# Kernel optimization log

Measured on AMD Instinct MI355X. Metric: run time of the kernel, lower is better.

Reference implementation:

```python
import jax, jax.numpy as jnp
import numpy as np

B, L, D, H = 2, 2048, 2048, 16
C = D // H  # head dim = 128
EPS = 1e-5


def setup_inputs() -> dict:
    key = jax.random.key(0)
    k1, k2, k3, k4 = jax.random.split(key, 4)
    scale = 1.0 / np.sqrt(D)
    return {
        "x": jax.random.normal(k1, (B, L, D), dtype=jnp.float32),
        "theta": jax.random.uniform(k2, (B, L, D // 2), dtype=jnp.float32) * 6.2831853,
        "w_qkv": jax.random.normal(k3, (3 * D, D), dtype=jnp.float32) * scale,
        "w_y": jax.random.normal(k4, (D, D), dtype=jnp.float32) * scale,
        "b_y": jnp.zeros((D,), dtype=jnp.float32),
    }


def _rms_norm(t):
    # RMSNorm over last dim, eps=1e-5, no affine
    return t * jax.lax.rsqrt(jnp.mean(t * t, axis=-1, keepdims=True) + EPS)


def _apply_rope(q, k, theta):
    # q, k: (B, H, L, C); theta: (B, H, L, C//2)
    qr, qi = q[..., 0::2], q[..., 1::2]
    kr, ki = k[..., 0::2], k[..., 1::2]
    cos_t, sin_t = jnp.cos(theta), jnp.sin(theta)
    q_rot = jnp.stack((qr * cos_t - qi * sin_t, qr * sin_t + qi * cos_t), axis=-1).reshape(q.shape)
    k_rot = jnp.stack((kr * cos_t - ki * sin_t, kr * sin_t + ki * cos_t), axis=-1).reshape(k.shape)
    return q_rot, k_rot


def reference(x, theta, w_qkv, w_y, b_y):
    # QKV projection: (B, L, 3D)
    qkv = jnp.einsum("bld,ed->ble", x, w_qkv)
    # rearrange '... L (n H C) -> n ... H L C'
    qkv = qkv.reshape(B, L, 3, H, C).transpose(2, 0, 3, 1, 4)  # (3, B, H, L, C)
    q, k, v = qkv[0], qkv[1], qkv[2]
    q, k = _rms_norm(q), _rms_norm(k)
    # theta: (B, L, H*C/2) -> (B, H, L, C/2)
    th = theta.reshape(B, L, H, C // 2).transpose(0, 2, 1, 3)
    q, k = _apply_rope(q, k, th)
    # scaled dot-product attention
    scores = jnp.einsum("bhqc,bhkc->bhqk", q, k) / np.sqrt(C).astype(np.float32)
    attn = jax.nn.softmax(scores, axis=-1)
    y = jnp.einsum("bhqk,bhkc->bhqc", attn, v)
    # (B, H, L, C) -> (B, L, H*C)
    y = y.transpose(0, 2, 1, 3).reshape(B, L, D)
    return jnp.einsum("bld,ed->ble", y, w_y) + b_y
```

## Files before the change

kernel.cpp:

```cpp
#include <hip/hip_runtime.h>
#include <stdint.h>

typedef uint16_t u16;
typedef __attribute__((ext_vector_type(8))) short bf16x8;
typedef __attribute__((ext_vector_type(4))) float f32x4;


__device__ __forceinline__ u16 f2bf(float f) {
  uint32_t u = __builtin_bit_cast(uint32_t, f);
  u += 0x7fffu + ((u >> 16) & 1u);
  return (u16)(u >> 16);
}
__device__ __forceinline__ float bf2f(u16 h) {
  return __builtin_bit_cast(float, (uint32_t)h << 16);
}
__device__ __forceinline__ uint32_t pack2bf(float a, float b) {
  uint32_t ua = __builtin_bit_cast(uint32_t, a) + 0x7fffu;
  uint32_t ub = __builtin_bit_cast(uint32_t, b) + 0x7fffu;
  return (ua >> 16) | (ub & 0xffff0000u);
}
__device__ __forceinline__ void gl_lds16(const u16* g, u16* l) {
  __builtin_amdgcn_global_load_lds((const __attribute__((address_space(1))) uint32_t*)g,
                                   (__attribute__((address_space(3))) uint32_t*)l, 16, 0, 0);
}

__global__ __launch_bounds__(256) void castk(const float* __restrict__ in,
                                             u16* __restrict__ out, int n) {
  int idx = (blockIdx.x * 256 + threadIdx.x) * 4;
  int stride = gridDim.x * 256 * 4;
  for (int i = idx; i < n; i += stride) {
    float4 v = *(const float4*)(in + i);
    uint32_t lo = (uint32_t)f2bf(v.x) | ((uint32_t)f2bf(v.y) << 16);
    uint32_t hi = (uint32_t)f2bf(v.z) | ((uint32_t)f2bf(v.w) << 16);
    *(uint2*)(out + i) = make_uint2(lo, hi);
  }
}

__global__ __launch_bounds__(512, 1) void gemm8_qkv(
    const u16* __restrict__ A, const u16* __restrict__ Bw,
    u16* __restrict__ qb, u16* __restrict__ kb, u16* __restrict__ vt) {
  __shared__ u16 sm[57344];
  const int K = 2048;
  const int tid = threadIdx.x, lane = tid & 63;
  const int wid = tid >> 6, g = lane >> 4, lr = lane & 15;
  const int wm = wid >> 2, wn = wid & 3;
  const int m0 = blockIdx.y * 256, n0 = blockIdx.x * 192;
  const int srow = tid >> 3, sjs = (tid & 7) ^ (srow & 7);

  auto stA = [&](int buf, int kt, int R) {
    gl_lds16(A + (size_t)(m0 + R + srow) * K + kt * 64 + sjs * 8,
             &sm[buf * 28672 + R * 64 + tid * 8]);
  };
  auto stB = [&](int buf, int kt, int R) {
    gl_lds16(Bw + (size_t)(n0 + R + srow) * K + kt * 64 + sjs * 8,
             &sm[buf * 28672 + 16384 + R * 64 + tid * 8]);
  };
  auto rdA = [&](const u16* As, int mf, int ks) {
    int ra = wm * 128 + mf * 16 + lr;
    return *(const bf16x8*)&As[ra * 64 + (((ks * 4 + g) ^ (ra & 7)) * 8)];
  };
  auto rdB = [&](const u16* Bs, int nf, int ks) {
    int rb = wn * 48 + nf * 16 + lr;
    return *(const bf16x8*)&Bs[rb * 64 + (((ks * 4 + g) ^ (rb & 7)) * 8)];
  };

  f32x4 acc[8][3] = {};
  bf16x8 bc[3][2], fP0[4][2], fP1[4][2];

  stB(0, 0, 0); stB(0, 0, 64); stB(0, 0, 128);
  stA(0, 0, 0); stA(0, 0, 128);
  stA(0, 0, 64); stA(0, 0, 192);
  asm volatile("s_waitcnt vmcnt(2)" ::: "memory");
  __builtin_amdgcn_s_barrier();
  {
    const u16* As0 = &sm[0];
#pragma unroll
    for (int i = 0; i < 4; ++i)
#pragma unroll
      for (int ks = 0; ks < 2; ++ks) fP0[i][ks] = rdA(As0, i, ks);
  }

  for (int t = 0; t < 32; ++t) {
    const int cur = t & 1, nxt = cur ^ 1;
    const int kn = (t < 31) ? t + 1 : 31;
    const u16* Asc = &sm[cur * 28672];
    const u16* Bsc = &sm[cur * 28672 + 16384];
    const u16* Asn = &sm[nxt * 28672];

    stB(nxt, kn, 0); stB(nxt, kn, 64); stB(nxt, kn, 128);
    stA(nxt, kn, 0); stA(nxt, kn, 128);
    asm volatile("s_waitcnt vmcnt(5)" ::: "memory");
    __builtin_amdgcn_s_barrier();
#pragma unroll
    for (int nf = 0; nf < 3; ++nf)
#pragma unroll
      for (int ks = 0; ks < 2; ++ks) bc[nf][ks] = rdB(Bsc, nf, ks);
#pragma unroll
    for (int i = 0; i < 4; ++i)
#pragma unroll
      for (int ks = 0; ks < 2; ++ks) fP1[i][ks] = rdA(Asc, 4 + i, ks);
    __builtin_amdgcn_s_setprio(1);
#pragma unroll
    for (int i = 0; i < 4; ++i)
#pragma unroll
      for (int nf = 0; nf < 3; ++nf) {
        acc[i][nf] = __builtin_amdgcn_mfma_f32_16x16x32_bf16(
            fP0[i][0], bc[nf][0], acc[i][nf], 0, 0, 0);
        acc[i][nf] = __builtin_amdgcn_mfma_f32_16x16x32_bf16(
            fP0[i][1], bc[nf][1], acc[i][nf], 0, 0, 0);
      }
    __builtin_amdgcn_s_setprio(0);

    stA(nxt, kn, 64); stA(nxt, kn, 192);
    asm volatile("s_waitcnt vmcnt(2)" ::: "memory");
    __builtin_amdgcn_s_barrier();
#pragma unroll
    for (int i = 0; i < 4; ++i)
#pragma unroll
      for (int ks = 0; ks < 2; ++ks) fP0[i][ks] = rdA(Asn, i, ks);
    __builtin_amdgcn_s_setprio(1);
#pragma unroll
    for (int i = 0; i < 4; ++i)
#pragma unroll
      for (int nf = 0; nf < 3; ++nf) {
        acc[4 + i][nf] = __builtin_amdgcn_mfma_f32_16x16x32_bf16(
            fP1[i][0], bc[nf][0], acc[4 + i][nf], 0, 0, 0);
        acc[4 + i][nf] = __builtin_amdgcn_mfma_f32_16x16x32_bf16(
            fP1[i][1], bc[nf][1], acc[4 + i][nf], 0, 0, 0);
      }
    __builtin_amdgcn_s_setprio(0);
  }
  asm volatile("s_waitcnt vmcnt(0)" ::: "memory");

#pragma unroll
  for (int mf = 0; mf < 8; ++mf)
#pragma unroll
    for (int nf = 0; nf < 3; ++nf) {
      int n = n0 + wn * 48 + nf * 16 + lr;
      int s = n >> 11, h = (n >> 7) & 15, cb = n & 127;
#pragma unroll
      for (int r = 0; r < 4; ++r) {
        int m = m0 + wm * 128 + mf * 16 + g * 4 + r;
        int b = m >> 11, lp = m & 2047;
        u16 val = f2bf(acc[mf][nf][r]);
        if (s == 0)
          qb[(size_t)((b * 16 + h) * 2048 + lp) * 128 + cb] = val;
        else if (s == 1)
          kb[(size_t)((b * 16 + h) * 2048 + lp) * 128 + cb] = val;
        else
          vt[(size_t)((b * 16 + h) * 128 + cb) * 2048 + lp] = val;
      }
    }
}

__global__ __launch_bounds__(256) void gemm_out(
    const u16* __restrict__ A, const u16* __restrict__ Bw, int K,
    float* __restrict__ out, const float* __restrict__ bias) {
  __shared__ u16 As[128 * 64];
  __shared__ u16 Bs[128 * 64];
  const int tid = threadIdx.x;
  const int lane = tid & 63, wid = tid >> 6;
  const int g = lane >> 4, lr = lane & 15;
  const int wm = wid >> 1, wn = wid & 1;
  const int m0 = blockIdx.y * 128, n0 = blockIdx.x * 128;
  f32x4 acc[4][4] = {};
  const int nk = K >> 6;
  for (int kt = 0; kt < nk; ++kt) {
    const int kbase = kt * 64;
#pragma unroll
    for (int i = 0; i < 4; ++i) {
      int ci = wid * 256 + i * 64 + lane;
      int row = ci >> 3, j = ci & 7;
      int js = j ^ (row & 7);
      gl_lds16(A + (size_t)(m0 + row) * K + kbase + js * 8, &As[(wid * 256 + i * 64) * 8]);
    }
#pragma unroll
    for (int i = 0; i < 4; ++i) {
      int ci = wid * 256 + i * 64 + lane;
      int row = ci >> 3, j = ci & 7;
      int js = j ^ (row & 7);
      gl_lds16(Bw + (size_t)(n0 + row) * K + kbase + js * 8, &Bs[(wid * 256 + i * 64) * 8]);
    }
    __syncthreads();
#pragma unroll
    for (int ks = 0; ks < 2; ++ks) {
      bf16x8 af[4], bfr[4];
#pragma unroll
      for (int t = 0; t < 4; ++t) {
        int ra = wm * 64 + t * 16 + lr;
        af[t] = *(const bf16x8*)&As[ra * 64 + (((ks * 4 + g) ^ (ra & 7)) * 8)];
        int rb = wn * 64 + t * 16 + lr;
        bfr[t] = *(const bf16x8*)&Bs[rb * 64 + (((ks * 4 + g) ^ (rb & 7)) * 8)];
      }
#pragma unroll
      for (int mt = 0; mt < 4; ++mt)
#pragma unroll
        for (int nt = 0; nt < 4; ++nt)
          acc[mt][nt] =
              __builtin_amdgcn_mfma_f32_16x16x32_bf16(af[mt], bfr[nt], acc[mt][nt], 0, 0, 0);
    }
    __syncthreads();
  }
#pragma unroll
  for (int mt = 0; mt < 4; ++mt)
#pragma unroll
    for (int nt = 0; nt < 4; ++nt) {
      int n = n0 + wn * 64 + nt * 16 + lr;
      float bv = bias[n];
#pragma unroll
      for (int r = 0; r < 4; ++r) {
        int m = m0 + wm * 64 + mt * 16 + g * 4 + r;
        out[(size_t)m * 2048 + n] = acc[mt][nt][r] + bv;
      }
    }
}

__global__ __launch_bounds__(256) void qk_fix(u16* __restrict__ qb, u16* __restrict__ kb,
                                              const float* __restrict__ theta) {
  const int row = blockIdx.x * 4 + (threadIdx.x >> 6);
  const int lane = threadIdx.x & 63;
  const int bh = row >> 11, l = row & 2047;
  const int b = bh >> 4, h = bh & 15;
  float th = theta[(size_t)(b * 2048 + l) * 1024 + h * 64 + lane];
  float sn, cs;
  __sincosf(th, &sn, &cs);
#pragma unroll
  for (int which = 0; which < 2; ++which) {
    u16* buf = which ? kb : qb;
    uint32_t* p = (uint32_t*)(buf + (size_t)row * 128) + lane;
    uint32_t v = *p;
    float x0 = bf2f((u16)(v & 0xffff)), x1 = bf2f((u16)(v >> 16));
    float ss = x0 * x0 + x1 * x1;
#pragma unroll
    for (int m = 1; m <= 32; m <<= 1) ss += __shfl_xor(ss, m);
    float rn = rsqrtf(ss * (1.0f / 128.0f) + 1e-5f);
    if (which == 0) rn *= 0.12751743f;
    x0 *= rn;
    x1 *= rn;
    float y0 = x0 * cs - x1 * sn;
    float y1 = x0 * sn + x1 * cs;
    *p = (uint32_t)f2bf(y0) | ((uint32_t)f2bf(y1) << 16);
  }
}

__global__ __launch_bounds__(512, 1) void attn_k(const u16* __restrict__ qb,
                                                 const u16* __restrict__ kb,
                                                 const u16* __restrict__ vt,
                                                 u16* __restrict__ yb) {
  __shared__ u16 sm[32768];
  const int gid = blockIdx.x;
  const int bh = (gid & 7) * 4 + ((gid >> 3) & 3);
  const int qtile = gid >> 5;
  const int b = bh >> 4, h = bh & 15;
  const int tid = threadIdx.x, lane = tid & 63, wid = tid >> 6;
  const int g = lane >> 4, lr = lane & 15;
  const int q0 = qtile * 256 + wid * 32;

  bf16x8 qf[2][4];
#pragma unroll
  for (int qs = 0; qs < 2; ++qs) {
    const u16* qrow = qb + (size_t)(bh * 2048 + q0 + qs * 16 + lr) * 128;
#pragma unroll
    for (int ks = 0; ks < 4; ++ks) qf[qs][ks] = *(const bf16x8*)&qrow[ks * 32 + g * 8];
  }

  auto stage = [&](int buf, int kv) {
#pragma unroll
    for (int i = 0; i < 2; ++i) {
      int ci = i * 512 + tid;
      int row = ci >> 4, j = ci & 15;
      gl_lds16(kb + (size_t)(bh * 2048 + kv + row) * 128 + (j ^ (row & 7)) * 8,
               &sm[buf * 8192 + ci * 8]);
    }
#pragma unroll
    for (int i = 0; i < 2; ++i) {
      int ci = i * 512 + tid;
      int row = ci >> 3, j = ci & 7;
      gl_lds16(vt + (size_t)(bh * 128 + row) * 2048 + kv + (j ^ (row & 7)) * 8,
               &sm[16384 + buf * 8192 + ci * 8]);
    }
  };

  f32x4 acc[2][8] = {};
  float mrun[2] = {-1e30f, -1e30f}, lrun[2] = {0.f, 0.f};
  const int sA = (2 * (g & 1)) * 16 + lr, sB = sA + 16;
  const bool hi2 = (g >> 1) != 0;

  stage(0, 0);
  asm volatile("s_waitcnt vmcnt(0)" ::: "memory");
  __builtin_amdgcn_s_barrier();

  for (int t = 0; t < 32; ++t) {
    const int cur = t & 1;
    if (t < 31) stage(cur ^ 1, (t + 1) * 64);
    const u16* Ks = &sm[cur * 8192];
    const u16* Vs = &sm[16384 + cur * 8192];

    f32x4 st[2][4] = {};
#pragma unroll
    for (int ks = 0; ks < 4; ++ks) {
      bf16x8 kf[4];
#pragma unroll
      for (int kt = 0; kt < 4; ++kt) {
        int row = kt * 16 + lr;
        kf[kt] = *(const bf16x8*)&Ks[row * 128 + (((ks * 4 + g) ^ (row & 7)) * 8)];
      }
#pragma unroll
      for (int kt = 0; kt < 4; ++kt)
#pragma unroll
        for (int qs = 0; qs < 2; ++qs)
          st[qs][kt] =
              __builtin_amdgcn_mfma_f32_16x16x32_bf16(kf[kt], qf[qs][ks], st[qs][kt], 0, 0, 0);
    }

    float pmax[2];
#pragma unroll
    for (int qs = 0; qs < 2; ++qs) {
      float m01 = fmaxf(fmaxf(st[qs][0][0], st[qs][0][1]), fmaxf(st[qs][0][2], st[qs][0][3]));
      float m23 = fmaxf(fmaxf(st[qs][1][0], st[qs][1][1]), fmaxf(st[qs][1][2], st[qs][1][3]));
      float m45 = fmaxf(fmaxf(st[qs][2][0], st[qs][2][1]), fmaxf(st[qs][2][2], st[qs][2][3]));
      float m67 = fmaxf(fmaxf(st[qs][3][0], st[qs][3][1]), fmaxf(st[qs][3][2], st[qs][3][3]));
      float mx = fmaxf(fmaxf(m01, m23), fmaxf(m45, m67));
      mx = fmaxf(mx, __shfl_xor(mx, 16));
      mx = fmaxf(mx, __shfl_xor(mx, 32));
      pmax[qs] = mx;
    }
    float need = fmaxf(pmax[0] - mrun[0], pmax[1] - mrun[1]);
    if (!__all(need <= 8.0f)) {
#pragma unroll
      for (int qs = 0; qs < 2; ++qs) {
        float mnew = fmaxf(mrun[qs], pmax[qs]);
        float corr = __builtin_amdgcn_exp2f(mrun[qs] - mnew);
        lrun[qs] *= corr;
        mrun[qs] = mnew;
#pragma unroll
        for (int ct = 0; ct < 8; ++ct) {
          acc[qs][ct][0] *= corr;
          acc[qs][ct][1] *= corr;
          acc[qs][ct][2] *= corr;
          acc[qs][ct][3] *= corr;
        }
      }
    }
    uint32_t pw[2][4][2];
#pragma unroll
    for (int qs = 0; qs < 2; ++qs) {
      float rsum = 0.f;
#pragma unroll
      for (int kt = 0; kt < 4; ++kt)
#pragma unroll
        for (int hf = 0; hf < 2; ++hf) {
          float e0 = __builtin_amdgcn_exp2f(st[qs][kt][2 * hf] - mrun[qs]);
          float e1 = __builtin_amdgcn_exp2f(st[qs][kt][2 * hf + 1] - mrun[qs]);
          rsum += e0 + e1;
          pw[qs][kt][hf] = pack2bf(e0, e1);
        }
      rsum += __shfl_xor(rsum, 16);
      rsum += __shfl_xor(rsum, 32);
      lrun[qs] += rsum;
    }

#pragma unroll
    for (int ks2 = 0; ks2 < 2; ++ks2) {
      bf16x8 pf[2];
#pragma unroll
      for (int qs = 0; qs < 2; ++qs) {
        uint32_t a0 = __shfl(pw[qs][ks2 * 2][0], sA);
        uint32_t a1 = __shfl(pw[qs][ks2 * 2][1], sA);
        uint32_t a2 = __shfl(pw[qs][ks2 * 2][0], sB);
        uint32_t a3 = __shfl(pw[qs][ks2 * 2][1], sB);
        uint32_t b0 = __shfl(pw[qs][ks2 * 2 + 1][0], sA);
        uint32_t b1 = __shfl(pw[qs][ks2 * 2 + 1][1], sA);
        uint32_t b2 = __shfl(pw[qs][ks2 * 2 + 1][0], sB);
        uint32_t b3 = __shfl(pw[qs][ks2 * 2 + 1][1], sB);
        union {
          uint32_t u[4];
          bf16x8 v;
        } tt;
        tt.u[0] = hi2 ? b0 : a0;
        tt.u[1] = hi2 ? b1 : a1;
        tt.u[2] = hi2 ? b2 : a2;
        tt.u[3] = hi2 ? b3 : a3;
        pf[qs] = tt.v;
      }
#pragma unroll
      for (int ct = 0; ct < 8; ++ct) {
        int row = ct * 16 + lr;
        bf16x8 vf = *(const bf16x8*)&Vs[row * 64 + (((ks2 * 4 + g) ^ (row & 7)) * 8)];
#pragma unroll
        for (int qs = 0; qs < 2; ++qs)
          acc[qs][ct] = __builtin_amdgcn_mfma_f32_16x16x32_bf16(vf, pf[qs], acc[qs][ct], 0, 0, 0);
      }
    }
    if (t < 31) {
      asm volatile("s_waitcnt vmcnt(0)" ::: "memory");
      __builtin_amdgcn_s_barrier();
    }
  }

#pragma unroll
  for (int qs = 0; qs < 2; ++qs) {
    float inv = 1.f / lrun[qs];
    const size_t orow = (size_t)(b * 2048 + q0 + qs * 16 + lr) * 2048 + h * 128;
#pragma unroll
    for (int ct = 0; ct < 8; ++ct) {
      uint32_t lo = pack2bf(acc[qs][ct][0] * inv, acc[qs][ct][1] * inv);
      uint32_t hi = pack2bf(acc[qs][ct][2] * inv, acc[qs][ct][3] * inv);
      *(uint2*)&yb[orow + ct * 16 + g * 4] = make_uint2(lo, hi);
    }
  }
}

extern "C" void kernel_launch(void* const* d_in, const int* in_sizes, int n_in,
                              void* d_out, int out_size, void* d_ws, size_t ws_size,
                              hipStream_t stream) {
  const float* x = (const float*)d_in[0];
  const float* theta = (const float*)d_in[1];
  const float* wqkv = (const float*)d_in[2];
  const float* wy = (const float*)d_in[3];
  const float* by = (const float*)d_in[4];
  float* out = (float*)d_out;
  char* ws = (char*)d_ws;
  u16* xb  = (u16*)(ws + 0);
  u16* wqb = (u16*)(ws + 16777216);
  u16* wyb = (u16*)(ws + 41943040);
  u16* qb  = (u16*)(ws + 50331648);
  u16* kb  = (u16*)(ws + 67108864);
  u16* vt  = (u16*)(ws + 83886080);
  u16* yb  = (u16*)(ws + 100663296);

  castk<<<2048, 256, 0, stream>>>(x, xb, 2 * 2048 * 2048);
  castk<<<2048, 256, 0, stream>>>(wqkv, wqb, 3 * 2048 * 2048);
  castk<<<1024, 256, 0, stream>>>(wy, wyb, 2048 * 2048);

  gemm8_qkv<<<dim3(32, 16), 512, 0, stream>>>(xb, wqb, qb, kb, vt);
  qk_fix<<<16384, 256, 0, stream>>>(qb, kb, theta);
  attn_k<<<256, 512, 0, stream>>>(qb, kb, vt, yb);
  gemm_out<<<dim3(16, 32), 256, 0, stream>>>(yb, wyb, 2048, out, by);
}
```

Baseline: 293.8 us.

## Pipeline output GEMM with split-phase double buffering; triple-buffer attention K/V

```diff
diff --git a/kernel.cpp b/kernel.cpp
--- a/kernel.cpp
+++ b/kernel.cpp
@@ -153,64 +153,112 @@
     }
 }
 
-__global__ __launch_bounds__(256) void gemm_out(
-    const u16* __restrict__ A, const u16* __restrict__ Bw, int K,
+__global__ __launch_bounds__(512, 1) void gemm_out(
+    const u16* __restrict__ A, const u16* __restrict__ Bw,
     float* __restrict__ out, const float* __restrict__ bias) {
-  __shared__ u16 As[128 * 64];
-  __shared__ u16 Bs[128 * 64];
-  const int tid = threadIdx.x;
-  const int lane = tid & 63, wid = tid >> 6;
-  const int g = lane >> 4, lr = lane & 15;
-  const int wm = wid >> 1, wn = wid & 1;
-  const int m0 = blockIdx.y * 128, n0 = blockIdx.x * 128;
-  f32x4 acc[4][4] = {};
-  const int nk = K >> 6;
-  for (int kt = 0; kt < nk; ++kt) {
-    const int kbase = kt * 64;
-#pragma unroll
-    for (int i = 0; i < 4; ++i) {
-      int ci = wid * 256 + i * 64 + lane;
-      int row = ci >> 3, j = ci & 7;
-      int js = j ^ (row & 7);
-      gl_lds16(A + (size_t)(m0 + row) * K + kbase + js * 8, &As[(wid * 256 + i * 64) * 8]);
-    }
-#pragma unroll
-    for (int i = 0; i < 4; ++i) {
-      int ci = wid * 256 + i * 64 + lane;
-      int row = ci >> 3, j = ci & 7;
-      int js = j ^ (row & 7);
-      gl_lds16(Bw + (size_t)(n0 + row) * K + kbase + js * 8, &Bs[(wid * 256 + i * 64) * 8]);
-    }
-    __syncthreads();
-#pragma unroll
-    for (int ks = 0; ks < 2; ++ks) {
-      bf16x8 af[4], bfr[4];
-#pragma unroll
-      for (int t = 0; t < 4; ++t) {
-        int ra = wm * 64 + t * 16 + lr;
-        af[t] = *(const bf16x8*)&As[ra * 64 + (((ks * 4 + g) ^ (ra & 7)) * 8)];
-        int rb = wn * 64 + t * 16 + lr;
-        bfr[t] = *(const bf16x8*)&Bs[rb * 64 + (((ks * 4 + g) ^ (rb & 7)) * 8)];
-      }
-#pragma unroll
-      for (int mt = 0; mt < 4; ++mt)
-#pragma unroll
-        for (int nt = 0; nt < 4; ++nt)
-          acc[mt][nt] =
-              __builtin_amdgcn_mfma_f32_16x16x32_bf16(af[mt], bfr[nt], acc[mt][nt], 0, 0, 0);
-    }
-    __syncthreads();
-  }
-#pragma unroll
-  for (int mt = 0; mt < 4; ++mt)
-#pragma unroll
-    for (int nt = 0; nt < 4; ++nt) {
-      int n = n0 + wn * 64 + nt * 16 + lr;
+  __shared__ u16 sm[49152];
+  const int K = 2048;
+  const int tid = threadIdx.x, lane = tid & 63;
+  const int wid = tid >> 6, g = lane >> 4, lr = lane & 15;
+  const int wm = wid >> 2, wn = wid & 3;
+  const int m0 = blockIdx.y * 256, n0 = blockIdx.x * 128;
+  const int srow = tid >> 3, sjs = (tid & 7) ^ (srow & 7);
+
+  auto stA = [&](int buf, int kt, int R) {
+    gl_lds16(A + (size_t)(m0 + R + srow) * K + kt * 64 + sjs * 8,
+             &sm[buf * 24576 + R * 64 + tid * 8]);
+  };
+  auto stB = [&](int buf, int kt, int R) {
+    gl_lds16(Bw + (size_t)(n0 + R + srow) * K + kt * 64 + sjs * 8,
+             &sm[buf * 24576 + 16384 + R * 64 + tid * 8]);
+  };
+  auto rdA = [&](const u16* As, int mf, int ks) {
+    int ra = wm * 128 + mf * 16 + lr;
+    return *(const bf16x8*)&As[ra * 64 + (((ks * 4 + g) ^ (ra & 7)) * 8)];
+  };
+  auto rdB = [&](const u16* Bs, int nf, int ks) {
+    int rb = wn * 32 + nf * 16 + lr;
+    return *(const bf16x8*)&Bs[rb * 64 + (((ks * 4 + g) ^ (rb & 7)) * 8)];
+  };
+
+  f32x4 acc[8][2] = {};
+  bf16x8 bc[2][2], fP0[4][2], fP1[4][2];
+
+  stB(0, 0, 0); stB(0, 0, 64);
+  stA(0, 0, 0); stA(0, 0, 128);
+  stA(0, 0, 64); stA(0, 0, 192);
+  asm volatile("s_waitcnt vmcnt(2)" ::: "memory");
+  __builtin_amdgcn_s_barrier();
+  {
+    const u16* As0 = &sm[0];
+#pragma unroll
+    for (int i = 0; i < 4; ++i)
+#pragma unroll
+      for (int ks = 0; ks < 2; ++ks) fP0[i][ks] = rdA(As0, i, ks);
+  }
+
+  for (int t = 0; t < 32; ++t) {
+    const int cur = t & 1, nxt = cur ^ 1;
+    const int kn = (t < 31) ? t + 1 : 31;
+    const u16* Asc = &sm[cur * 24576];
+    const u16* Bsc = &sm[cur * 24576 + 16384];
+    const u16* Asn = &sm[nxt * 24576];
+
+    stB(nxt, kn, 0); stB(nxt, kn, 64);
+    stA(nxt, kn, 0); stA(nxt, kn, 128);
+    asm volatile("s_waitcnt vmcnt(4)" ::: "memory");
+    __builtin_amdgcn_s_barrier();
+#pragma unroll
+    for (int nf = 0; nf < 2; ++nf)
+#pragma unroll
+      for (int ks = 0; ks < 2; ++ks) bc[nf][ks] = rdB(Bsc, nf, ks);
+#pragma unroll
+    for (int i = 0; i < 4; ++i)
+#pragma unroll
+      for (int ks = 0; ks < 2; ++ks) fP1[i][ks] = rdA(Asc, 4 + i, ks);
+    __builtin_amdgcn_s_setprio(1);
+#pragma unroll
+    for (int i = 0; i < 4; ++i)
+#pragma unroll
+      for (int nf = 0; nf < 2; ++nf) {
+        acc[i][nf] = __builtin_amdgcn_mfma_f32_16x16x32_bf16(
+            fP0[i][0], bc[nf][0], acc[i][nf], 0, 0, 0);
+        acc[i][nf] = __builtin_amdgcn_mfma_f32_16x16x32_bf16(
+            fP0[i][1], bc[nf][1], acc[i][nf], 0, 0, 0);
+      }
+    __builtin_amdgcn_s_setprio(0);
+
+    stA(nxt, kn, 64); stA(nxt, kn, 192);
+    asm volatile("s_waitcnt vmcnt(2)" ::: "memory");
+    __builtin_amdgcn_s_barrier();
+#pragma unroll
+    for (int i = 0; i < 4; ++i)
+#pragma unroll
+      for (int ks = 0; ks < 2; ++ks) fP0[i][ks] = rdA(Asn, i, ks);
+    __builtin_amdgcn_s_setprio(1);
+#pragma unroll
+    for (int i = 0; i < 4; ++i)
+#pragma unroll
+      for (int nf = 0; nf < 2; ++nf) {
+        acc[4 + i][nf] = __builtin_amdgcn_mfma_f32_16x16x32_bf16(
+            fP1[i][0], bc[nf][0], acc[4 + i][nf], 0, 0, 0);
+        acc[4 + i][nf] = __builtin_amdgcn_mfma_f32_16x16x32_bf16(
+            fP1[i][1], bc[nf][1], acc[4 + i][nf], 0, 0, 0);
+      }
+    __builtin_amdgcn_s_setprio(0);
+  }
+  asm volatile("s_waitcnt vmcnt(0)" ::: "memory");
+
+#pragma unroll
+  for (int mf = 0; mf < 8; ++mf)
+#pragma unroll
+    for (int nf = 0; nf < 2; ++nf) {
+      int n = n0 + wn * 32 + nf * 16 + lr;
       float bv = bias[n];
 #pragma unroll
       for (int r = 0; r < 4; ++r) {
-        int m = m0 + wm * 64 + mt * 16 + g * 4 + r;
-        out[(size_t)m * 2048 + n] = acc[mt][nt][r] + bv;
+        int m = m0 + wm * 128 + mf * 16 + g * 4 + r;
+        out[(size_t)m * 2048 + n] = acc[mf][nf][r] + bv;
       }
     }
 }
@@ -247,7 +295,7 @@
                                                  const u16* __restrict__ kb,
                                                  const u16* __restrict__ vt,
                                                  u16* __restrict__ yb) {
-  __shared__ u16 sm[32768];
+  __shared__ u16 sm[49152];
   const int gid = blockIdx.x;
   const int bh = (gid & 7) * 4 + ((gid >> 3) & 3);
   const int qtile = gid >> 5;
@@ -277,7 +325,7 @@
       int ci = i * 512 + tid;
       int row = ci >> 3, j = ci & 7;
       gl_lds16(vt + (size_t)(bh * 128 + row) * 2048 + kv + (j ^ (row & 7)) * 8,
-               &sm[16384 + buf * 8192 + ci * 8]);
+               &sm[24576 + buf * 8192 + ci * 8]);
     }
   };
 
@@ -287,14 +335,19 @@
   const bool hi2 = (g >> 1) != 0;
 
   stage(0, 0);
-  asm volatile("s_waitcnt vmcnt(0)" ::: "memory");
+  stage(1, 64);
+  asm volatile("s_waitcnt vmcnt(4)" ::: "memory");
   __builtin_amdgcn_s_barrier();
 
+  int cur = 0;
   for (int t = 0; t < 32; ++t) {
-    const int cur = t & 1;
-    if (t < 31) stage(cur ^ 1, (t + 1) * 64);
+    if (t < 31) {
+      int nb = (cur == 0) ? 2 : cur - 1;
+      int kvn = ((t < 30) ? t + 2 : 31) * 64;
+      stage(nb, kvn);
+    }
     const u16* Ks = &sm[cur * 8192];
-    const u16* Vs = &sm[16384 + cur * 8192];
+    const u16* Vs = &sm[24576 + cur * 8192];
 
     f32x4 st[2][4] = {};
 #pragma unroll
@@ -393,10 +446,12 @@
       }
     }
     if (t < 31) {
-      asm volatile("s_waitcnt vmcnt(0)" ::: "memory");
+      asm volatile("s_waitcnt vmcnt(4)" ::: "memory");
       __builtin_amdgcn_s_barrier();
     }
-  }
+    cur = (cur == 2) ? 0 : cur + 1;
+  }
+  asm volatile("s_waitcnt vmcnt(0)" ::: "memory");
 
 #pragma unroll
   for (int qs = 0; qs < 2; ++qs) {
@@ -436,5 +491,5 @@
   gemm8_qkv<<<dim3(32, 16), 512, 0, stream>>>(xb, wqb, qb, kb, vt);
   qk_fix<<<16384, 256, 0, stream>>>(qb, kb, theta);
   attn_k<<<256, 512, 0, stream>>>(qb, kb, vt, yb);
-  gemm_out<<<dim3(16, 32), 256, 0, stream>>>(yb, wyb, 2048, out, by);
-}
+  gemm_out<<<dim3(16, 16), 512, 0, stream>>>(yb, wyb, out, by);
+}
```

New measurement: 285.1 us. 3.0% less time.
